# Kernel tuning notes

Hardware: AMD Instinct MI355X
Metric: run time of the kernel (lower is better)

The kernel has to match this reference:

```python
import jax, jax.numpy as jnp
import numpy as np

B, I, S, H, O = 128, 64, 2048, 128, 64


def setup_inputs() -> dict:
    key = jax.random.key(0)
    ks = jax.random.split(key, 9)
    sc = 0.1
    return {
        "x": jax.random.normal(ks[0], (B, I, S), dtype=jnp.float32),
        "Wx_out": jax.random.normal(ks[1], (I, 4 * H), dtype=jnp.float32) * sc,
        "Wh_out": jax.random.normal(ks[2], (H, 4 * H), dtype=jnp.float32) * sc,
        "b_out": jnp.zeros((4 * H,), dtype=jnp.float32),
        "Wx_in": jax.random.normal(ks[3], (H, 4 * H), dtype=jnp.float32) * sc,
        "Wh_in": jax.random.normal(ks[4], (H, 4 * H), dtype=jnp.float32) * sc,
        "b_in": jnp.zeros((4 * H,), dtype=jnp.float32),
        "W_lin": jax.random.normal(ks[5], (O, H), dtype=jnp.float32) * 0.01,
        "b_lin": jnp.zeros((O,), dtype=jnp.float32),
    }


def reference(x, Wx_out, Wh_out, b_out, Wx_in, Wh_in, b_in, W_lin, b_lin):
    # x: (B, I, S) -> permute(0,2,1) -> (B, S, I); scan over time axis.
    xs = jnp.transpose(x, (2, 0, 1))  # (S, B, I)
    h0 = jnp.zeros((x.shape[0], Wh_out.shape[0]), dtype=x.dtype)

    def step(carry, xt):
        h, c, cn = carry  # outer hidden, outer cell, inner cell
        gates = xt @ Wx_out + h @ Wh_out + b_out
        i, f, o, g = jnp.split(gates, 4, axis=-1)
        i, f, o = jax.nn.sigmoid(i), jax.nn.sigmoid(f), jax.nn.sigmoid(o)
        g = jnp.tanh(g)
        x_in = i * g          # inner LSTM input
        h_in = f * c          # inner LSTM hidden
        gi = x_in @ Wx_in + h_in @ Wh_in + b_in
        ii, fi, oi, gg = jnp.split(gi, 4, axis=-1)
        cn_new = jax.nn.sigmoid(fi) * cn + jax.nn.sigmoid(ii) * jnp.tanh(gg)
        c_new = jax.nn.sigmoid(oi) * jnp.tanh(cn_new)  # outer cell = inner hidden
        h_new = o * jnp.tanh(c_new)
        return (h_new, c_new, cn_new), h_new

    _, hs = jax.lax.scan(step, (h0, h0, h0), xs)  # hs: (S, B, H)
    hs = jnp.transpose(hs, (1, 0, 2))             # (B, S, H)
    return hs @ W_lin.T + b_lin                   # (B, S, O)
```

## Files before the change

kernel.cpp:

```cpp
#include <hip/hip_runtime.h>
#include <hip/hip_fp16.h>

#define BB 128
#define II 64
#define SS 2048
#define HH 128
#define GG 512
#define OO 64

typedef _Float16 f16x2 __attribute__((ext_vector_type(2)));
union F4H { float4 f4; f16x2 h[4]; };

__device__ __forceinline__ f16x2 pack2(float a, float b) {
    f16x2 r; r.x = (_Float16)a; r.y = (_Float16)b; return r;
}

__device__ __forceinline__ float dot2(f16x2 w, f16x2 v, float c) {
#if __has_builtin(__builtin_amdgcn_fdot2)
    return __builtin_amdgcn_fdot2(w, v, c, false);
#else
    return fmaf((float)w.x, (float)v.x, fmaf((float)w.y, (float)v.y, c));
#endif
}

__device__ __forceinline__ float tanh_f(float v) {
    float a = fabsf(v);
    float e = __expf(-2.0f * a);
    float r = (1.0f - e) * __builtin_amdgcn_rcpf(1.0f + e);
    return v < 0.0f ? -r : r;
}

template<int C>
__device__ __forceinline__ float qb(float v) {
    return __int_as_float(__builtin_amdgcn_mov_dpp(
        __float_as_int(v), 0x55 * C, 0xF, 0xF, true));
}
__device__ __forceinline__ float xor4(float v) {
    return __int_as_float(__builtin_amdgcn_ds_swizzle(__float_as_int(v), 0x101F));
}

__global__ void __launch_bounds__(512)
__attribute__((amdgpu_waves_per_eu(2)))
nlstm_scan(
    const float* __restrict__ x,
    const float* __restrict__ Wx_out, const float* __restrict__ Wh_out,
    const float* __restrict__ b_out,
    const float* __restrict__ Wx_in, const float* __restrict__ Wh_in,
    const float* __restrict__ b_in,
    const float* __restrict__ W_lin, const float* __restrict__ b_lin,
    float* __restrict__ out)
{
    const int b = blockIdx.x;
    const int j = threadIdx.x;
    const int u = j >> 2;
    const int g = j & 3;
    const int jcol = g * HH + u;

    __shared__ __align__(16) float4 wxf[8 * 512];
    __shared__ __align__(16) f16x2 xb[2][II / 2];
    __shared__ __align__(16) f16x2 hb[HH / 2];
    __shared__ __align__(16) f16x2 xib[HH / 2];
    __shared__ __align__(16) f16x2 hib[HH / 2];

    f16x2 who[HH / 2];
    f16x2 wxi[HH / 2];
    f16x2 whi[HH / 2];
#pragma unroll
    for (int m = 0; m < HH / 2; ++m)
        who[m] = pack2(Wh_out[(2 * m) * GG + jcol], Wh_out[(2 * m + 1) * GG + jcol]);
#pragma unroll
    for (int m = 0; m < HH / 2; ++m)
        wxi[m] = pack2(Wx_in[(2 * m) * GG + jcol], Wx_in[(2 * m + 1) * GG + jcol]);
#pragma unroll
    for (int m = 0; m < HH / 2; ++m)
        whi[m] = pack2(Wh_in[(2 * m) * GG + jcol], Wh_in[(2 * m + 1) * GG + jcol]);

    const float bo  = b_out[jcol];
    const float bi2 = b_in[jcol];
    const int   pn = j >> 3;
    const int   ps = j & 7;
    const float bl = b_lin[pn];

    F4H wl[2];
#pragma unroll
    for (int q = 0; q < 2; ++q) {
        const int c = 2 * ps + q;
#pragma unroll
        for (int r = 0; r < 4; ++r)
            wl[q].h[r] = pack2(W_lin[pn * HH + 8 * c + 2 * r],
                               W_lin[pn * HH + 8 * c + 2 * r + 1]);
    }

#pragma unroll
    for (int c = 0; c < 8; ++c) {
        F4H w4;
#pragma unroll
        for (int q = 0; q < 4; ++q)
            w4.h[q] = pack2(Wx_out[(8 * c + 2 * q) * GG + jcol],
                            Wx_out[(8 * c + 2 * q + 1) * GG + jcol]);
        wxf[c * 512 + j] = w4.f4;
    }

    const float* xrow = x + (size_t)b * II * SS;
    float* orow = out + (size_t)b * SS * OO;

    if (j < II / 2) xb[0][j] = pack2(xrow[(2 * j) * SS], xrow[(2 * j + 1) * SS]);
    if (j < HH / 2) hb[j] = pack2(0.f, 0.f);
    __syncthreads();

    float c_reg = 0.f, cn_reg = 0.f;

    const float4* hb4 = (const float4*)hb;
    const float4* xi4 = (const float4*)xib;
    const float4* hi4 = (const float4*)hib;
    const bool isT = (g == 3);

#pragma unroll 1
    for (int t = 0; t < SS; ++t) {
        const int cur = t & 1;

        float xa = 0.f, xc = 0.f;
        const int tn = (t + 1 < SS) ? t + 1 : t;
        if (j < II / 2) {
            xa = xrow[(2 * j) * SS + tn];
            xc = xrow[(2 * j + 1) * SS + tn];
        }

        const float4* xc4 = (const float4*)xb[cur];
        float a0 = 0.f, a1 = 0.f, a2 = 0.f, a3 = 0.f;
#pragma unroll
        for (int c = 0; c < 8; ++c) {
            F4H xu; xu.f4 = xc4[c];
            F4H wu; wu.f4 = wxf[c * 512 + j];
            a0 = dot2(wu.h[0], xu.h[0], a0);
            a1 = dot2(wu.h[1], xu.h[1], a1);
            a2 = dot2(wu.h[2], xu.h[2], a2);
            a3 = dot2(wu.h[3], xu.h[3], a3);
        }
#pragma unroll
        for (int c = 0; c < 16; ++c) {
            F4H hu; hu.f4 = hb4[c];
            a0 = dot2(who[4 * c + 0], hu.h[0], a0);
            a1 = dot2(who[4 * c + 1], hu.h[1], a1);
            a2 = dot2(who[4 * c + 2], hu.h[2], a2);
            a3 = dot2(who[4 * c + 3], hu.h[3], a3);
        }
        float acc = ((a0 + a1) + (a2 + a3)) + bo;

        float ap = isT ? 2.f * acc : acc;
        float s  = __builtin_amdgcn_rcpf(1.f + __expf(-ap));
        float av = isT ? fmaf(2.f, s, -1.f) : s;

        float vi = qb<0>(av), vf = qb<1>(av), vo = qb<2>(av), vg = qb<3>(av);
        float x_in    = vi * vg;
        float h_in    = vf * c_reg;
        float o_outer = vo;

        float p0 = 0.f, p1 = 0.f;
        {
            F4H hu0; hu0.f4 = hb4[2 * ps];
            F4H hu1; hu1.f4 = hb4[2 * ps + 1];
            p0 = dot2(wl[0].h[0], hu0.h[0], p0);
            p1 = dot2(wl[0].h[1], hu0.h[1], p1);
            p0 = dot2(wl[0].h[2], hu0.h[2], p0);
            p1 = dot2(wl[0].h[3], hu0.h[3], p1);
            p0 = dot2(wl[1].h[0], hu1.h[0], p0);
            p1 = dot2(wl[1].h[1], hu1.h[1], p1);
            p0 = dot2(wl[1].h[2], hu1.h[2], p0);
            p1 = dot2(wl[1].h[3], hu1.h[3], p1);
        }
        float p = p0 + p1;
        p += __shfl_down(p, 4, 8);
        p += __shfl_down(p, 2, 8);
        p += __shfl_down(p, 1, 8);
        if (ps == 0 && t > 0) orow[(size_t)(t - 1) * OO + pn] = p + bl;

        float xin_n = xor4(x_in);
        float hin_n = xor4(h_in);
        if ((j & 7) == 0) {
            xib[u >> 1] = pack2(x_in, xin_n);
            hib[u >> 1] = pack2(h_in, hin_n);
        }
        __syncthreads();

        float b0 = 0.f, b1 = 0.f, b2 = 0.f, b3 = 0.f;
#pragma unroll
        for (int c = 0; c < 16; ++c) {
            F4H xu; xu.f4 = xi4[c];
            b0 = dot2(wxi[4 * c + 0], xu.h[0], b0);
            b1 = dot2(wxi[4 * c + 1], xu.h[1], b1);
            b2 = dot2(wxi[4 * c + 2], xu.h[2], b2);
            b3 = dot2(wxi[4 * c + 3], xu.h[3], b3);
        }
#pragma unroll
        for (int c = 0; c < 16; ++c) {
            F4H hu; hu.f4 = hi4[c];
            b0 = dot2(whi[4 * c + 0], hu.h[0], b0);
            b1 = dot2(whi[4 * c + 1], hu.h[1], b1);
            b2 = dot2(whi[4 * c + 2], hu.h[2], b2);
            b3 = dot2(whi[4 * c + 3], hu.h[3], b3);
        }
        float acc2 = ((b0 + b1) + (b2 + b3)) + bi2;

        float ap2 = isT ? 2.f * acc2 : acc2;
        float s2  = __builtin_amdgcn_rcpf(1.f + __expf(-ap2));
        float av2 = isT ? fmaf(2.f, s2, -1.f) : s2;

        float ii = qb<0>(av2), fi = qb<1>(av2), oi = qb<2>(av2), gg = qb<3>(av2);
        float cn_new = fmaf(fi, cn_reg, ii * gg);
        cn_reg = cn_new;
        float c_new = oi * tanh_f(cn_new);
        c_reg = c_new;
        float h_new = o_outer * tanh_f(c_new);

        float hn_n = xor4(h_new);
        if ((j & 7) == 0) hb[u >> 1] = pack2(h_new, hn_n);
        if (j < II / 2) xb[cur ^ 1][j] = pack2(xa, xc);
        __syncthreads();
    }

    {
        float p0 = 0.f, p1 = 0.f;
        F4H hu0; hu0.f4 = hb4[2 * ps];
        F4H hu1; hu1.f4 = hb4[2 * ps + 1];
        p0 = dot2(wl[0].h[0], hu0.h[0], p0);
        p1 = dot2(wl[0].h[1], hu0.h[1], p1);
        p0 = dot2(wl[0].h[2], hu0.h[2], p0);
        p1 = dot2(wl[0].h[3], hu0.h[3], p1);
        p0 = dot2(wl[1].h[0], hu1.h[0], p0);
        p1 = dot2(wl[1].h[1], hu1.h[1], p1);
        p0 = dot2(wl[1].h[2], hu1.h[2], p0);
        p1 = dot2(wl[1].h[3], hu1.h[3], p1);
        float p = p0 + p1;
        p += __shfl_down(p, 4, 8);
        p += __shfl_down(p, 2, 8);
        p += __shfl_down(p, 1, 8);
        if (ps == 0) orow[(size_t)(SS - 1) * OO + pn] = p + bl;
    }
}

extern "C" void kernel_launch(void* const* d_in, const int* in_sizes, int n_in,
                              void* d_out, int out_size, void* d_ws, size_t ws_size,
                              hipStream_t stream) {
    (void)in_sizes; (void)n_in; (void)d_ws; (void)ws_size; (void)out_size;
    const float* x      = (const float*)d_in[0];
    const float* Wx_out = (const float*)d_in[1];
    const float* Wh_out = (const float*)d_in[2];
    const float* b_out  = (const float*)d_in[3];
    const float* Wx_in  = (const float*)d_in[4];
    const float* Wh_in  = (const float*)d_in[5];
    const float* b_in   = (const float*)d_in[6];
    const float* W_lin  = (const float*)d_in[7];
    const float* b_lin  = (const float*)d_in[8];
    float* out = (float*)d_out;

    nlstm_scan<<<dim3(BB), dim3(512), 0, stream>>>(
        x, Wx_out, Wh_out, b_out, Wx_in, Wh_in, b_in, W_lin, b_lin, out);
}
```

Baseline: 4.286 ms.

## Batch x prefetch into 16-step LDS tiles, use DPP rotates and raw barriers

Instead of every step loading the next x column with strided global reads by 32 threads, all 512 threads each load one element every 16 steps into a double-buffered transposed LDS tile covering 16 timesteps. Cross-lane reductions and neighbour exchanges switch from shfl/ds_swizzle to DPP row-rotate moves, and __syncthreads is replaced by an inline s_waitcnt lgkmcnt(0) + s_barrier. The aim is to take global-load latency off the serial recurrence and cut LDS-based shuffle traffic. The raw barrier does not wait on vmcnt, which is fine here because the barriers only order LDS accesses.

```diff
diff --git a/kernel.cpp b/kernel.cpp
--- a/kernel.cpp
+++ b/kernel.cpp
@@ -35,8 +35,14 @@
     return __int_as_float(__builtin_amdgcn_mov_dpp(
         __float_as_int(v), 0x55 * C, 0xF, 0xF, true));
 }
-__device__ __forceinline__ float xor4(float v) {
-    return __int_as_float(__builtin_amdgcn_ds_swizzle(__float_as_int(v), 0x101F));
+template<int N>
+__device__ __forceinline__ float rolN(float v) {
+    return __int_as_float(__builtin_amdgcn_mov_dpp(
+        __float_as_int(v), 0x120 + (16 - N), 0xF, 0xF, true));
+}
+
+__device__ __forceinline__ void barrier_lds() {
+    asm volatile("s_waitcnt lgkmcnt(0)\n\ts_barrier" ::: "memory");
 }
 
 __global__ void __launch_bounds__(512)
@@ -57,7 +63,7 @@
     const int jcol = g * HH + u;
 
     __shared__ __align__(16) float4 wxf[8 * 512];
-    __shared__ __align__(16) f16x2 xb[2][II / 2];
+    __shared__ __align__(16) f16x2 xt[2][16][36];
     __shared__ __align__(16) f16x2 hb[HH / 2];
     __shared__ __align__(16) f16x2 xib[HH / 2];
     __shared__ __align__(16) f16x2 hib[HH / 2];
@@ -104,7 +110,12 @@
     const float* xrow = x + (size_t)b * II * SS;
     float* orow = out + (size_t)b * SS * OO;
 
-    if (j < II / 2) xb[0][j] = pack2(xrow[(2 * j) * SS], xrow[(2 * j + 1) * SS]);
+    const int xm  = j >> 4;
+    const int xtl = j & 15;
+    const float* xg0 = xrow + (size_t)(2 * xm) * SS + xtl;
+    const float* xg1 = xrow + (size_t)(2 * xm + 1) * SS + xtl;
+
+    xt[0][xtl][xm] = pack2(xg0[0], xg1[0]);
     if (j < HH / 2) hb[j] = pack2(0.f, 0.f);
     __syncthreads();
 
@@ -115,18 +126,20 @@
     const float4* hi4 = (const float4*)hib;
     const bool isT = (g == 3);
 
+    float pr0 = 0.f, pr1 = 0.f;
+
 #pragma unroll 1
     for (int t = 0; t < SS; ++t) {
-        const int cur = t & 1;
-
-        float xa = 0.f, xc = 0.f;
-        const int tn = (t + 1 < SS) ? t + 1 : t;
-        if (j < II / 2) {
-            xa = xrow[(2 * j) * SS + tn];
-            xc = xrow[(2 * j + 1) * SS + tn];
-        }
-
-        const float4* xc4 = (const float4*)xb[cur];
+        const int stl = t & 15;
+        const int tb  = (t >> 4) & 1;
+
+        if (stl == 0) {
+            const int Tn = (t + 16 < SS) ? t + 16 : t;
+            pr0 = xg0[Tn];
+            pr1 = xg1[Tn];
+        }
+
+        const float4* xc4 = (const float4*)&xt[tb][stl][0];
         float a0 = 0.f, a1 = 0.f, a2 = 0.f, a3 = 0.f;
 #pragma unroll
         for (int c = 0; c < 8; ++c) {
@@ -170,18 +183,18 @@
             p1 = dot2(wl[1].h[3], hu1.h[3], p1);
         }
         float p = p0 + p1;
-        p += __shfl_down(p, 4, 8);
-        p += __shfl_down(p, 2, 8);
-        p += __shfl_down(p, 1, 8);
+        p += rolN<4>(p);
+        p += rolN<2>(p);
+        p += rolN<1>(p);
         if (ps == 0 && t > 0) orow[(size_t)(t - 1) * OO + pn] = p + bl;
 
-        float xin_n = xor4(x_in);
-        float hin_n = xor4(h_in);
+        float xin_n = rolN<4>(x_in);
+        float hin_n = rolN<4>(h_in);
         if ((j & 7) == 0) {
             xib[u >> 1] = pack2(x_in, xin_n);
             hib[u >> 1] = pack2(h_in, hin_n);
         }
-        __syncthreads();
+        barrier_lds();
 
         float b0 = 0.f, b1 = 0.f, b2 = 0.f, b3 = 0.f;
 #pragma unroll
@@ -213,10 +226,10 @@
         c_reg = c_new;
         float h_new = o_outer * tanh_f(c_new);
 
-        float hn_n = xor4(h_new);
+        float hn_n = rolN<4>(h_new);
         if ((j & 7) == 0) hb[u >> 1] = pack2(h_new, hn_n);
-        if (j < II / 2) xb[cur ^ 1][j] = pack2(xa, xc);
-        __syncthreads();
+        if (stl == 0) xt[tb ^ 1][xtl][xm] = pack2(pr0, pr1);
+        barrier_lds();
     }
 
     {
@@ -232,9 +245,9 @@
         p0 = dot2(wl[1].h[2], hu1.h[2], p0);
         p1 = dot2(wl[1].h[3], hu1.h[3], p1);
         float p = p0 + p1;
-        p += __shfl_down(p, 4, 8);
-        p += __shfl_down(p, 2, 8);
-        p += __shfl_down(p, 1, 8);
+        p += rolN<4>(p);
+        p += rolN<2>(p);
+        p += rolN<1>(p);
         if (ps == 0) orow[(size_t)(SS - 1) * OO + pn] = p + bl;
     }
 }
```

Measured after the change: 4.034 ms. -5.9%, faster.
